# Kernel optimization log

Hardware: AMD Instinct MI355X
Metric: run time of the kernel (lower is better)

Reference implementation:

```python
import jax, jax.numpy as jnp
import numpy as np

ARTIST_V = 16384
GENRE_V = 2048
TOTAL = ARTIST_V + GENRE_V + 1  # 18433
HIDDEN = TOTAL // 2            # 9216
OUT = 64
BATCH = 4096


def setup_inputs() -> dict:
    key = jax.random.key(0)
    k1, k2, k3, k4, k5, k6, k7 = jax.random.split(key, 7)
    artist_ids = jax.random.randint(k1, (BATCH,), 0, ARTIST_V, dtype=jnp.int64 if jax.config.jax_enable_x64 else jnp.int32)
    genre_ids = jax.random.randint(k2, (BATCH,), 0, GENRE_V, dtype=artist_ids.dtype)
    year_norms = jax.random.uniform(k3, (BATCH,), dtype=jnp.float32)
    s1 = 1.0 / np.sqrt(TOTAL)
    s2 = 1.0 / np.sqrt(HIDDEN)
    W1 = jax.random.uniform(k4, (HIDDEN, TOTAL), jnp.float32, -s1, s1)
    b1 = jax.random.uniform(k5, (HIDDEN,), jnp.float32, -s1, s1)
    W2 = jax.random.uniform(k6, (OUT, HIDDEN), jnp.float32, -s2, s2)
    b2 = jax.random.uniform(k7, (OUT,), jnp.float32, -s2, s2)
    return {"artist_ids": artist_ids, "genre_ids": genre_ids, "year_norms": year_norms,
            "W1": W1, "b1": b1, "W2": W2, "b2": b2}


def reference(artist_ids, genre_ids, year_norms, W1, b1, W2, b2):
    # one_hot(artist) @ W1[:, :A].T  ==  gather of W1 columns == gather of W1.T rows.
    # combined = [onehot(artist) | onehot(genre) | year] -> Linear -> ReLU -> Linear
    # (Dropout is identity at inference.)
    W1T = W1.T  # [TOTAL, HIDDEN]
    h = (W1T[artist_ids]                     # [B, HIDDEN] artist one-hot matmul
         + W1T[ARTIST_V + genre_ids]         # genre one-hot matmul
         + year_norms[:, None] * W1T[-1]     # year scalar column
         + b1)
    h = jax.nn.relu(h)
    return h @ W2.T + b2  # [B, OUT]
```

## Files before the change

### kernel.cpp

```cpp
#include <hip/hip_runtime.h>

#define ARTIST_V 16384
#define GENRE_V  2048
#define TOTAL    18433
#define HIDDEN   9216
#define OUT_D    64
#define BATCH    4096

typedef unsigned int  uint;
typedef unsigned short ushort;
typedef __attribute__((ext_vector_type(8))) short short8;
typedef __attribute__((ext_vector_type(4))) float f32x4;

__device__ __forceinline__ ushort f2bf(float f) {
    uint u = __float_as_uint(f);
    u += 0x7FFFu + ((u >> 16) & 1u);
    return (ushort)(u >> 16);
}
__device__ __forceinline__ float bf2f(ushort b) {
    return __uint_as_float(((uint)b) << 16);
}

__global__ __launch_bounds__(256) void k_init(const float* __restrict__ b2,
                                              float4* __restrict__ out4) {
    int idx = blockIdx.x * 256 + threadIdx.x;
    const float4* b24 = (const float4*)b2;
    out4[idx] = b24[threadIdx.x & 15];
}

__global__ __launch_bounds__(256) void k_hidden(
    const int*   __restrict__ artist,
    const int*   __restrict__ genre,
    const float* __restrict__ year,
    const float* __restrict__ W1,
    const float* __restrict__ b1,
    uint4*       __restrict__ H2v)
{
    __shared__ ushort srow[TOTAL + 4];
    const int tid = threadIdx.x;
    const int hb  = blockIdx.x;
    const int h0  = hb * 8;

    uint res[16][4];
    #pragma unroll
    for (int j = 0; j < 16; j++) {
        res[j][0] = 0u; res[j][1] = 0u; res[j][2] = 0u; res[j][3] = 0u;
    }

    #pragma unroll
    for (int r = 0; r < 8; r++) {
        const int h = h0 + r;
        const size_t base = (size_t)h * TOTAL;
        const int t = (int)(base & 3);
        const int s = (4 - t) & 3;

        if (tid < s) srow[tid + t] = f2bf(W1[base + tid]);
        const int nvec = (TOTAL - s) >> 2;
        const float4* vp = (const float4*)(W1 + base + s);
        for (int j = tid; j < nvec; j += 256) {
            float4 v = vp[j];
            int o = s + t + 4 * j;
            uint2 packed;
            packed.x = (uint)f2bf(v.x) | ((uint)f2bf(v.y) << 16);
            packed.y = (uint)f2bf(v.z) | ((uint)f2bf(v.w) << 16);
            *(uint2*)(srow + o) = packed;
        }
        const int tail0 = s + 4 * nvec;
        const int ntail = TOTAL - tail0;
        if (tid < ntail) srow[t + tail0 + tid] = f2bf(W1[base + tail0 + tid]);
        __syncthreads();

        const float yc  = bf2f(srow[t + TOTAL - 1]);
        const float b1h = b1[h];
        #pragma unroll
        for (int j = 0; j < 16; j++) {
            int b = tid + 256 * j;
            int a = artist[b];
            int g = genre[b];
            float y = year[b];
            float hv = bf2f(srow[t + a]) + bf2f(srow[t + ARTIST_V + g]) + y * yc + b1h;
            hv = fmaxf(hv, 0.0f);
            res[j][r >> 1] |= ((uint)f2bf(hv)) << ((r & 1) * 16);
        }
        __syncthreads();
    }

    const size_t obase = (size_t)hb * BATCH;
    #pragma unroll
    for (int j = 0; j < 16; j++) {
        int b = tid + 256 * j;
        uint4 v;
        v.x = res[j][0]; v.y = res[j][1]; v.z = res[j][2]; v.w = res[j][3];
        H2v[obase + b] = v;
    }
}

__global__ __launch_bounds__(256) void k_gemm(
    const uint4* __restrict__ H2v,
    const float* __restrict__ W2,
    float*       __restrict__ out)
{
    const int lane = threadIdx.x & 63;
    const int wv   = threadIdx.x >> 6;
    const int l15  = lane & 15;
    const int lhi  = lane >> 4;
    const int m0   = blockIdx.x * 64 + wv * 16;
    const int k0   = blockIdx.y * 512;

    f32x4 acc[4];
    #pragma unroll
    for (int n = 0; n < 4; n++) acc[n] = (f32x4){0.f, 0.f, 0.f, 0.f};

    for (int k = k0; k < k0 + 512; k += 32) {
        uint4 av = H2v[(size_t)((k >> 3) + lhi) * BATCH + (m0 + l15)];
        union { uint4 u; short8 s; } ua; ua.u = av;
        short8 afrag = ua.s;

        const float* wbase = W2 + (size_t)l15 * HIDDEN + (k + lhi * 8);
        #pragma unroll
        for (int n = 0; n < 4; n++) {
            const float* wp = wbase + (size_t)(n * 16) * HIDDEN;
            float4 w0 = *(const float4*)wp;
            float4 w1 = *(const float4*)(wp + 4);
            short8 bfrag;
            bfrag[0] = (short)f2bf(w0.x); bfrag[1] = (short)f2bf(w0.y);
            bfrag[2] = (short)f2bf(w0.z); bfrag[3] = (short)f2bf(w0.w);
            bfrag[4] = (short)f2bf(w1.x); bfrag[5] = (short)f2bf(w1.y);
            bfrag[6] = (short)f2bf(w1.z); bfrag[7] = (short)f2bf(w1.w);
            acc[n] = __builtin_amdgcn_mfma_f32_16x16x32_bf16(afrag, bfrag, acc[n], 0, 0, 0);
        }
    }

    #pragma unroll
    for (int n = 0; n < 4; n++) {
        #pragma unroll
        for (int r = 0; r < 4; r++) {
            int row = m0 + lhi * 4 + r;
            int col = n * 16 + l15;
            atomicAdd(&out[(size_t)row * OUT_D + col], acc[n][r]);
        }
    }
}

extern "C" void kernel_launch(void* const* d_in, const int* in_sizes, int n_in,
                              void* d_out, int out_size, void* d_ws, size_t ws_size,
                              hipStream_t stream) {
    const int*   artist = (const int*)d_in[0];
    const int*   genre  = (const int*)d_in[1];
    const float* year   = (const float*)d_in[2];
    const float* W1     = (const float*)d_in[3];
    const float* b1     = (const float*)d_in[4];
    const float* W2     = (const float*)d_in[5];
    const float* b2     = (const float*)d_in[6];
    float* out = (float*)d_out;
    uint4* H2v = (uint4*)d_ws;

    k_init  <<<256, 256, 0, stream>>>(b2, (float4*)out);
    k_hidden<<<1152, 256, 0, stream>>>(artist, genre, year, W1, b1, H2v);
    k_gemm  <<<dim3(64, 18), 256, 0, stream>>>((const uint4*)H2v, W2, out);
}
```

Measured before the change: 1.051 ms.

## Prefetch next W1 row into registers, pre-convert W2, split-K with a reduction

The hidden kernel now uses 512 threads and 6 rows per block. It keeps artist/genre ids and years in registers. It prefetches the next W1 row into registers while the current row is consumed from LDS, so the global-load latency of the roughly 680 MB W1 stream overlaps with the gather work. W2 is converted to bf16 once in a small prep kernel, so the GEMM loads bf16 fragments directly. The GEMM uses 4-way split-K into a partial buffer, followed by a reduce kernel that adds b2, replacing the float atomics. The costs are more register pressure, extra launches, a larger workspace, and float4 loads from W1 row starts that are not 16-byte aligned.

After: 941.3 us. 1.12x faster.

```diff
diff --git a/kernel.cpp b/kernel.cpp
--- a/kernel.cpp
+++ b/kernel.cpp
@@ -7,7 +7,16 @@
 #define OUT_D    64
 #define BATCH    4096
 
-typedef unsigned int  uint;
+#define ROWS_PB  6
+#define NBLK     (HIDDEN / ROWS_PB)
+#define THR      512
+#define SEG      (TOTAL - 1)
+#define PF_N     (SEG / 4 / THR)
+
+#define KSPLIT   4
+#define KCHUNK   (HIDDEN / KSPLIT)
+
+typedef unsigned int   uint;
 typedef unsigned short ushort;
 typedef __attribute__((ext_vector_type(8))) short short8;
 typedef __attribute__((ext_vector_type(4))) float f32x4;
@@ -21,125 +30,152 @@
     return __uint_as_float(((uint)b) << 16);
 }
 
-__global__ __launch_bounds__(256) void k_init(const float* __restrict__ b2,
-                                              float4* __restrict__ out4) {
-    int idx = blockIdx.x * 256 + threadIdx.x;
-    const float4* b24 = (const float4*)b2;
-    out4[idx] = b24[threadIdx.x & 15];
-}
-
-__global__ __launch_bounds__(256) void k_hidden(
+__global__ __launch_bounds__(256) void k_prep(const float* __restrict__ W2,
+                                              ushort* __restrict__ W2b) {
+    int t = blockIdx.x * 256 + threadIdx.x;
+    float4 v = *(const float4*)(W2 + (size_t)t * 4);
+    uint2 p;
+    p.x = (uint)f2bf(v.x) | ((uint)f2bf(v.y) << 16);
+    p.y = (uint)f2bf(v.z) | ((uint)f2bf(v.w) << 16);
+    *(uint2*)(W2b + (size_t)t * 4) = p;
+}
+
+__global__ __launch_bounds__(THR) void k_hidden(
     const int*   __restrict__ artist,
     const int*   __restrict__ genre,
     const float* __restrict__ year,
     const float* __restrict__ W1,
     const float* __restrict__ b1,
-    uint4*       __restrict__ H2v)
+    uint*        __restrict__ H2p)
 {
-    __shared__ ushort srow[TOTAL + 4];
+    __shared__ ushort srow[SEG];
     const int tid = threadIdx.x;
     const int hb  = blockIdx.x;
-    const int h0  = hb * 8;
-
-    uint res[16][4];
-    #pragma unroll
-    for (int j = 0; j < 16; j++) {
-        res[j][0] = 0u; res[j][1] = 0u; res[j][2] = 0u; res[j][3] = 0u;
-    }
-
-    #pragma unroll
-    for (int r = 0; r < 8; r++) {
+    const int h0  = hb * ROWS_PB;
+
+    uint  ag[8]; float yv[8];
+    #pragma unroll
+    for (int j = 0; j < 8; j++) {
+        int b = tid + THR * j;
+        ag[j] = (uint)artist[b] | ((uint)genre[b] << 16);
+        yv[j] = year[b];
+    }
+
+    uint res[8][3];
+    #pragma unroll
+    for (int j = 0; j < 8; j++) { res[j][0] = 0u; res[j][1] = 0u; res[j][2] = 0u; }
+
+    float4 pf[PF_N];
+    {
+        const float4* vp = (const float4*)(W1 + (size_t)h0 * TOTAL);
+        #pragma unroll
+        for (int i = 0; i < PF_N; i++) pf[i] = vp[i * THR + tid];
+        #pragma unroll
+        for (int i = 0; i < PF_N; i++) {
+            uint2 p;
+            p.x = (uint)f2bf(pf[i].x) | ((uint)f2bf(pf[i].y) << 16);
+            p.y = (uint)f2bf(pf[i].z) | ((uint)f2bf(pf[i].w) << 16);
+            *(uint2*)(srow + (i * THR + tid) * 4) = p;
+        }
+        __syncthreads();
+    }
+
+    #pragma unroll
+    for (int r = 0; r < ROWS_PB; r++) {
         const int h = h0 + r;
-        const size_t base = (size_t)h * TOTAL;
-        const int t = (int)(base & 3);
-        const int s = (4 - t) & 3;
-
-        if (tid < s) srow[tid + t] = f2bf(W1[base + tid]);
-        const int nvec = (TOTAL - s) >> 2;
-        const float4* vp = (const float4*)(W1 + base + s);
-        for (int j = tid; j < nvec; j += 256) {
-            float4 v = vp[j];
-            int o = s + t + 4 * j;
-            uint2 packed;
-            packed.x = (uint)f2bf(v.x) | ((uint)f2bf(v.y) << 16);
-            packed.y = (uint)f2bf(v.z) | ((uint)f2bf(v.w) << 16);
-            *(uint2*)(srow + o) = packed;
-        }
-        const int tail0 = s + 4 * nvec;
-        const int ntail = TOTAL - tail0;
-        if (tid < ntail) srow[t + tail0 + tid] = f2bf(W1[base + tail0 + tid]);
-        __syncthreads();
-
-        const float yc  = bf2f(srow[t + TOTAL - 1]);
+        if (r + 1 < ROWS_PB) {
+            const float4* vp = (const float4*)(W1 + (size_t)(h + 1) * TOTAL);
+            #pragma unroll
+            for (int i = 0; i < PF_N; i++) pf[i] = vp[i * THR + tid];
+        }
+        const float yw  = W1[(size_t)h * TOTAL + SEG];
         const float b1h = b1[h];
         #pragma unroll
-        for (int j = 0; j < 16; j++) {
-            int b = tid + 256 * j;
-            int a = artist[b];
-            int g = genre[b];
-            float y = year[b];
-            float hv = bf2f(srow[t + a]) + bf2f(srow[t + ARTIST_V + g]) + y * yc + b1h;
+        for (int j = 0; j < 8; j++) {
+            int a = (int)(ag[j] & 0xFFFFu);
+            int g = (int)(ag[j] >> 16);
+            float hv = bf2f(srow[a]) + bf2f(srow[ARTIST_V + g]) + yv[j] * yw + b1h;
             hv = fmaxf(hv, 0.0f);
             res[j][r >> 1] |= ((uint)f2bf(hv)) << ((r & 1) * 16);
         }
         __syncthreads();
-    }
-
-    const size_t obase = (size_t)hb * BATCH;
-    #pragma unroll
-    for (int j = 0; j < 16; j++) {
-        int b = tid + 256 * j;
-        uint4 v;
-        v.x = res[j][0]; v.y = res[j][1]; v.z = res[j][2]; v.w = res[j][3];
-        H2v[obase + b] = v;
+        if (r + 1 < ROWS_PB) {
+            #pragma unroll
+            for (int i = 0; i < PF_N; i++) {
+                uint2 p;
+                p.x = (uint)f2bf(pf[i].x) | ((uint)f2bf(pf[i].y) << 16);
+                p.y = (uint)f2bf(pf[i].z) | ((uint)f2bf(pf[i].w) << 16);
+                *(uint2*)(srow + (i * THR + tid) * 4) = p;
+            }
+            __syncthreads();
+        }
+    }
+
+    #pragma unroll
+    for (int q = 0; q < 3; q++) {
+        size_t base = (size_t)(hb * 3 + q) * BATCH;
+        #pragma unroll
+        for (int j = 0; j < 8; j++) H2p[base + tid + THR * j] = res[j][q];
     }
 }
 
 __global__ __launch_bounds__(256) void k_gemm(
-    const uint4* __restrict__ H2v,
-    const float* __restrict__ W2,
-    float*       __restrict__ out)
+    const uint*   __restrict__ H2p,
+    const ushort* __restrict__ W2b,
+    float*        __restrict__ part)
 {
     const int lane = threadIdx.x & 63;
     const int wv   = threadIdx.x >> 6;
     const int l15  = lane & 15;
     const int lhi  = lane >> 4;
     const int m0   = blockIdx.x * 64 + wv * 16;
-    const int k0   = blockIdx.y * 512;
+    const int k0   = blockIdx.y * KCHUNK;
 
     f32x4 acc[4];
     #pragma unroll
     for (int n = 0; n < 4; n++) acc[n] = (f32x4){0.f, 0.f, 0.f, 0.f};
 
-    for (int k = k0; k < k0 + 512; k += 32) {
-        uint4 av = H2v[(size_t)((k >> 3) + lhi) * BATCH + (m0 + l15)];
-        union { uint4 u; short8 s; } ua; ua.u = av;
+    for (int kk = k0; kk < k0 + KCHUNK; kk += 32) {
+        int p0 = (kk >> 1) + lhi * 4;
+        union { uint u[4]; short8 s; } ua;
+        #pragma unroll
+        for (int q = 0; q < 4; q++)
+            ua.u[q] = H2p[(size_t)(p0 + q) * BATCH + m0 + l15];
         short8 afrag = ua.s;
 
-        const float* wbase = W2 + (size_t)l15 * HIDDEN + (k + lhi * 8);
+        const ushort* wb = W2b + (size_t)l15 * HIDDEN + kk + lhi * 8;
         #pragma unroll
         for (int n = 0; n < 4; n++) {
-            const float* wp = wbase + (size_t)(n * 16) * HIDDEN;
-            float4 w0 = *(const float4*)wp;
-            float4 w1 = *(const float4*)(wp + 4);
-            short8 bfrag;
-            bfrag[0] = (short)f2bf(w0.x); bfrag[1] = (short)f2bf(w0.y);
-            bfrag[2] = (short)f2bf(w0.z); bfrag[3] = (short)f2bf(w0.w);
-            bfrag[4] = (short)f2bf(w1.x); bfrag[5] = (short)f2bf(w1.y);
-            bfrag[6] = (short)f2bf(w1.z); bfrag[7] = (short)f2bf(w1.w);
+            short8 bfrag = *(const short8*)(wb + (size_t)(n * 16) * HIDDEN);
             acc[n] = __builtin_amdgcn_mfma_f32_16x16x32_bf16(afrag, bfrag, acc[n], 0, 0, 0);
         }
     }
 
+    float* pb = part + (size_t)blockIdx.y * (BATCH * OUT_D);
     #pragma unroll
     for (int n = 0; n < 4; n++) {
         #pragma unroll
-        for (int r = 0; r < 4; r++) {
-            int row = m0 + lhi * 4 + r;
-            int col = n * 16 + l15;
-            atomicAdd(&out[(size_t)row * OUT_D + col], acc[n][r]);
-        }
-    }
+        for (int r = 0; r < 4; r++)
+            pb[(size_t)(m0 + lhi * 4 + r) * OUT_D + n * 16 + l15] = acc[n][r];
+    }
+}
+
+__global__ __launch_bounds__(256) void k_reduce(const float* __restrict__ part,
+                                                const float* __restrict__ b2,
+                                                float4*      __restrict__ out4) {
+    int idx = blockIdx.x * 256 + threadIdx.x;
+    const float4* p = (const float4*)part;
+    float4 s0 = p[idx];
+    float4 s1 = p[idx + 65536];
+    float4 s2 = p[idx + 131072];
+    float4 s3 = p[idx + 196608];
+    float4 bb = ((const float4*)b2)[threadIdx.x & 15];
+    float4 o;
+    o.x = s0.x + s1.x + s2.x + s3.x + bb.x;
+    o.y = s0.y + s1.y + s2.y + s3.y + bb.y;
+    o.z = s0.z + s1.z + s2.z + s3.z + bb.z;
+    o.w = s0.w + s1.w + s2.w + s3.w + bb.w;
+    out4[idx] = o;
 }
 
 extern "C" void kernel_launch(void* const* d_in, const int* in_sizes, int n_in,
@@ -153,9 +189,14 @@
     const float* W2     = (const float*)d_in[5];
     const float* b2     = (const float*)d_in[6];
     float* out = (float*)d_out;
-    uint4* H2v = (uint4*)d_ws;
-
-    k_init  <<<256, 256, 0, stream>>>(b2, (float4*)out);
-    k_hidden<<<1152, 256, 0, stream>>>(artist, genre, year, W1, b1, H2v);
-    k_gemm  <<<dim3(64, 18), 256, 0, stream>>>((const uint4*)H2v, W2, out);
-}
+
+    char* ws = (char*)d_ws;
+    uint*   H2p = (uint*)ws;
+    ushort* W2b = (ushort*)(ws + 75497472);
+    float*  part = (float*)(ws + 75497472 + 1179648);
+
+    k_prep  <<<576, 256, 0, stream>>>(W2, W2b);
+    k_hidden<<<NBLK, THR, 0, stream>>>(artist, genre, year, W1, b1, H2p);
+    k_gemm  <<<dim3(BATCH / 64, KSPLIT), 256, 0, stream>>>(H2p, W2b, part);
+    k_reduce<<<256, 256, 0, stream>>>(part, b2, (float4*)out);
+}
```
